# Kernel optimization log

Hardware: AMD Instinct MI355X
Metric: run time of the kernel (lower is better)

The kernel has to match this reference:

```python
import jax
import jax.numpy as jnp
import numpy as np

# Module configuration (matches init_kwargs)
N, C, H, W = 8, 256, 64, 64
CO, KH, KW = 256, 3, 3
SH, SW = 1, 1
PH, PW = 1, 1
DH, DW = 1, 1
G, DG = 1, 1
K = KH * KW
HO = (H + 2 * PH - (DH * (KH - 1) + 1)) // SH + 1
WO = (W + 2 * PW - (DW * (KW - 1) + 1)) // SW + 1


def setup_inputs() -> dict:
    key = jax.random.key(0)
    k1, k2, k3, k4 = jax.random.split(key, 4)
    x = jax.random.normal(k1, (N, C, H, W), dtype=jnp.float32)
    offset = jax.random.normal(k2, (N, DG * 2 * K, HO, WO), dtype=jnp.float32)
    mask = jax.random.uniform(k3, (N, DG * K, HO, WO), dtype=jnp.float32)
    stdv = 1.0 / np.sqrt(C * KH * KW)
    weight = jax.random.uniform(k4, (CO, C // G, KH, KW), dtype=jnp.float32,
                                minval=-stdv, maxval=stdv)
    return {"x": x, "offset": offset, "mask": mask, "weight": weight}


def _deform_sample(x, offset, mask):
    """Modulated deformable bilinear sampling (DCNv2 im2col).

    Returns columns [N, C, K, HO, WO].
    """
    Cg = C // DG
    # offset layout: [N, DG, K, 2(y,x), HO, WO]
    off = offset.reshape(N, DG, K, 2, HO, WO)
    off_y, off_x = off[:, :, :, 0], off[:, :, :, 1]

    # Base sampling grid per kernel tap: [K, HO, WO] broadcastable
    kgy = (jnp.repeat(jnp.arange(KH), KW) * DH).astype(jnp.float32)  # [K]
    kgx = (jnp.tile(jnp.arange(KW), KH) * DW).astype(jnp.float32)    # [K]
    oy = (jnp.arange(HO) * SH - PH).astype(jnp.float32)              # [HO]
    ox = (jnp.arange(WO) * SW - PW).astype(jnp.float32)              # [WO]
    py = kgy[:, None, None] + oy[None, :, None] + off_y  # [N,DG,K,HO,WO]
    px = kgx[:, None, None] + ox[None, None, :] + off_x  # [N,DG,K,HO,WO]

    y0 = jnp.floor(py)
    x0 = jnp.floor(px)
    ly = py - y0
    lx = px - x0
    y0i = y0.astype(jnp.int32)
    x0i = x0.astype(jnp.int32)
    y1i = y0i + 1
    x1i = x0i + 1

    xf = x.reshape(N, DG, Cg, H * W)

    def gather_one(xf_nd, idx_nd):
        # xf_nd: [Cg, H*W], idx_nd: [K*HO*WO] -> [Cg, K*HO*WO]
        return xf_nd[:, idx_nd]

    gather = jax.vmap(jax.vmap(gather_one))  # over N, DG

    def corner(yi, xi, wgt):
        valid = (yi >= 0) & (yi < H) & (xi >= 0) & (xi < W)
        yc = jnp.clip(yi, 0, H - 1)
        xc = jnp.clip(xi, 0, W - 1)
        idx = (yc * W + xc).reshape(N, DG, K * HO * WO)
        g = gather(xf, idx).reshape(N, DG, Cg, K, HO, WO)
        w = (wgt * valid.astype(x.dtype))[:, :, None]  # [N,DG,1,K,HO,WO]
        return g * w

    cols = corner(y0i, x0i, (1.0 - ly) * (1.0 - lx))
    cols = cols + corner(y0i, x1i, (1.0 - ly) * lx)
    cols = cols + corner(y1i, x0i, ly * (1.0 - lx))
    cols = cols + corner(y1i, x1i, ly * lx)

    # modulation
    m = mask.reshape(N, DG, 1, K, HO, WO)
    cols = cols * m
    return cols.reshape(N, C, K, HO, WO)


def reference(x, offset, mask, weight):
    cols = _deform_sample(x, offset, mask)              # [N,C,K,HO,WO]
    colsg = cols.reshape(N, G, C // G, K, HO, WO)
    wg = weight.reshape(G, CO // G, C // G, K)
    out = jnp.einsum('ngckhw,gock->ngohw', colsg, wg)
    return out.reshape(N, CO, HO, WO)
```

## Files before the change

kernel.cpp:

```cpp
#include <hip/hip_runtime.h>
#include <hip/hip_bf16.h>
#include <stdint.h>

#define N_   8
#define C_   256
#define H_   64
#define W_   64
#define CO_  256
#define K_   9
#define HO_  64
#define WO_  64
#define CK_  (C_ * K_)
#define P_   (HO_ * WO_)

#define BN   64
#define BK   64
#define NT   36
#define NTHR 512

typedef __attribute__((ext_vector_type(8))) short bf16x8;
typedef __attribute__((ext_vector_type(4))) float f32x4;

__device__ __forceinline__ unsigned short f2bf(float f) {
    uint32_t u = __builtin_bit_cast(uint32_t, f);
    uint32_t r = (u + 0x7FFFu + ((u >> 16) & 1u)) >> 16;
    return (unsigned short)r;
}
__device__ __forceinline__ float bf2f(unsigned short u) {
    return __builtin_bit_cast(float, (uint32_t)u << 16);
}
__device__ __forceinline__ float h2f(unsigned short u) {
    return (float)__builtin_bit_cast(_Float16, u);
}
__device__ __forceinline__ unsigned short f2h(float f) {
    return __builtin_bit_cast(unsigned short, (_Float16)f);
}


__global__ __launch_bounds__(256)
void transpose_x(const float* __restrict__ x, unsigned short* __restrict__ xT) {
    __shared__ float t[64][65];
    const int n  = blockIdx.z;
    const int c0 = blockIdx.y * 64;
    const int h0 = blockIdx.x * 64;
    const int tx = threadIdx.x & 63;
    const int ty = threadIdx.x >> 6;
    const float* xp = x + ((size_t)n * C_ + c0) * P_ + h0;
    #pragma unroll
    for (int i = 0; i < 16; ++i) {
        int c = ty * 16 + i;
        t[c][tx] = xp[(size_t)c * P_ + tx];
    }
    __syncthreads();
    unsigned short* op = xT + ((size_t)n * P_ + h0) * C_ + c0;
    #pragma unroll
    for (int i = 0; i < 16; ++i) {
        int hw = ty * 16 + i;
        op[(size_t)hw * C_ + tx] = f2bf(t[tx][hw]);
    }
}

__global__ __launch_bounds__(256)
void reorder_w(const float* __restrict__ w, unsigned short* __restrict__ Wt) {
    const int co = blockIdx.x;
    const int c  = threadIdx.x;
    const float* src = w + (size_t)co * CK_ + (size_t)c * K_;
    float v[9];
    #pragma unroll
    for (int k = 0; k < 9; ++k) v[k] = src[k];
    #pragma unroll
    for (int k = 0; k < 9; ++k)
        Wt[(size_t)co * CK_ + k * C_ + c] = f2bf(v[k]);
}

__device__ __forceinline__ void barrier_lgkm_only() {
    __builtin_amdgcn_sched_barrier(0);
    asm volatile("s_waitcnt lgkmcnt(0)" ::: "memory");
    __builtin_amdgcn_s_barrier();
    __builtin_amdgcn_sched_barrier(0);
}

__global__ __launch_bounds__(NTHR, 4)
void dcn_main(const unsigned short* __restrict__ xT,
              const unsigned short* __restrict__ Wt,
              const float* __restrict__ offset,
              const float* __restrict__ mask,
              float* __restrict__ out) {
    __shared__ uint2  sIdx[BN * K_];
    __shared__ uint2  sW  [BN * K_];
    __shared__ unsigned short sWs[CO_ * BK];
    __shared__ unsigned short sBs[BN * BK];

    const int tid = threadIdx.x;
    const int bid = blockIdx.x;
    const int n   = bid & 7;
    const int p0  = (bid >> 3) * BN;

    for (int e = tid; e < BN * K_; e += NTHR) {
        int pl = e / K_;
        int k  = e - pl * K_;
        int p  = p0 + pl;
        int ho = p >> 6, wo = p & 63;
        float offy = offset[(size_t)((n * 2 * K_ + 2 * k)     * P_) + p];
        float offx = offset[(size_t)((n * 2 * K_ + 2 * k + 1) * P_) + p];
        float m    = mask  [(size_t)((n * K_ + k) * P_) + p];
        float py = (float)(k / 3 + ho - 1) + offy;
        float px = (float)(k % 3 + wo - 1) + offx;
        float y0f = floorf(py), x0f = floorf(px);
        float ly = py - y0f,   lx = px - x0f;
        int y0 = (int)y0f, x0 = (int)x0f;
        int y1 = y0 + 1,   x1 = x0 + 1;
        bool vy0 = (y0 >= 0) & (y0 < H_);
        bool vy1 = (y1 >= 0) & (y1 < H_);
        bool vx0 = (x0 >= 0) & (x0 < W_);
        bool vx1 = (x1 >= 0) & (x1 < W_);
        float w00 = (1.f - ly) * (1.f - lx) * m * ((vy0 & vx0) ? 1.f : 0.f);
        float w01 = (1.f - ly) * lx         * m * ((vy0 & vx1) ? 1.f : 0.f);
        float w10 = ly * (1.f - lx)         * m * ((vy1 & vx0) ? 1.f : 0.f);
        float w11 = ly * lx                 * m * ((vy1 & vx1) ? 1.f : 0.f);
        unsigned int cy0 = (unsigned)min(max(y0, 0), H_ - 1);
        unsigned int cy1 = (unsigned)min(max(y1, 0), H_ - 1);
        unsigned int cx0 = (unsigned)min(max(x0, 0), W_ - 1);
        unsigned int cx1 = (unsigned)min(max(x1, 0), W_ - 1);
        sIdx[e] = make_uint2((cy0 * W_ + cx0) | ((cy0 * W_ + cx1) << 16),
                             (cy1 * W_ + cx0) | ((cy1 * W_ + cx1) << 16));
        sW[e]   = make_uint2((unsigned)f2h(w00) | ((unsigned)f2h(w01) << 16),
                             (unsigned)f2h(w10) | ((unsigned)f2h(w11) << 16));
    }
    __syncthreads();

    const unsigned short* xTn = xT + (size_t)n * P_ * C_;

    const int spl = tid >> 3;
    const int cs8 = (tid & 7) * 8;
    char* bdst = (char*)sBs + spl * 128 + ((((tid & 7)) ^ (spl & 7)) << 4);
    const int wco  = tid >> 1;
    const int wchq = (tid & 1) * 4;
    const int wswz = wco & 7;
    char* wrow = (char*)sWs + wco * 128;
    const unsigned short* wsrcbase = Wt + (size_t)wco * CK_ + (tid & 1) * 32;

    const int lane = tid & 63;
    const int wid  = tid >> 6;
    const int wm   = (wid & 3) * 64;
    const int wp   = (wid >> 2) * 32;
    const int l15  = lane & 15;
    const int l4   = lane >> 4;
    const int slA  = l4 ^ (l15 & 7);

    f32x4 acc[4][2] = {};

    uint4 qa, qb, qc, qd;
    uint4 wq0, wq1, wq2, wq3;

    {
        const unsigned short* ws = wsrcbase;
        wq0 = *(const uint4*)(ws);
        wq1 = *(const uint4*)(ws + 8);
        wq2 = *(const uint4*)(ws + 16);
        wq3 = *(const uint4*)(ws + 24);
        uint2 id = sIdx[spl * K_];
        const unsigned short* base = xTn + cs8;
        qa = *(const uint4*)(base + ((size_t)(id.x & 0xFFFFu) << 8));
        qb = *(const uint4*)(base + ((size_t)(id.x >> 16)     << 8));
        qc = *(const uint4*)(base + ((size_t)(id.y & 0xFFFFu) << 8));
        qd = *(const uint4*)(base + ((size_t)(id.y >> 16)     << 8));
    }

    for (int t = 0; t < NT; ++t) {
        const int k = t >> 2;

        barrier_lgkm_only();

        asm volatile("s_waitcnt vmcnt(0)" ::: "memory");

        {
            *(uint4*)(wrow + (((wchq + 0) ^ wswz) << 4)) = wq0;
            *(uint4*)(wrow + (((wchq + 1) ^ wswz) << 4)) = wq1;
            *(uint4*)(wrow + (((wchq + 2) ^ wswz) << 4)) = wq2;
            *(uint4*)(wrow + (((wchq + 3) ^ wswz) << 4)) = wq3;

            uint2 wv = sW[spl * K_ + k];
            float w0 = h2f((unsigned short)(wv.x & 0xFFFF));
            float w1 = h2f((unsigned short)(wv.x >> 16));
            float w2 = h2f((unsigned short)(wv.y & 0xFFFF));
            float w3 = h2f((unsigned short)(wv.y >> 16));
            const unsigned* pa = (const unsigned*)&qa;
            const unsigned* pb = (const unsigned*)&qb;
            const unsigned* pc = (const unsigned*)&qc;
            const unsigned* pd = (const unsigned*)&qd;
            unsigned rr[4];
            #pragma unroll
            for (int h = 0; h < 4; ++h) {
                unsigned ua = pa[h], ub = pb[h], uc = pc[h], ud = pd[h];
                float v0 = w0 * bf2f((unsigned short)(ua & 0xFFFF))
                         + w1 * bf2f((unsigned short)(ub & 0xFFFF))
                         + w2 * bf2f((unsigned short)(uc & 0xFFFF))
                         + w3 * bf2f((unsigned short)(ud & 0xFFFF));
                float v1 = w0 * bf2f((unsigned short)(ua >> 16))
                         + w1 * bf2f((unsigned short)(ub >> 16))
                         + w2 * bf2f((unsigned short)(uc >> 16))
                         + w3 * bf2f((unsigned short)(ud >> 16));
                asm("v_cvt_pk_bf16_f32 %0, %1, %2" : "=v"(rr[h]) : "v"(v0), "v"(v1));
            }
            *(uint4*)bdst = make_uint4(rr[0], rr[1], rr[2], rr[3]);
        }

        if (t + 1 < NT) {
            const int kn  = (t + 1) >> 2;
            const int c0n = ((t + 1) & 3) * 64;
            const unsigned short* ws = wsrcbase + kn * C_ + c0n;
            wq0 = *(const uint4*)(ws);
            wq1 = *(const uint4*)(ws + 8);
            wq2 = *(const uint4*)(ws + 16);
            wq3 = *(const uint4*)(ws + 24);
            uint2 id = sIdx[spl * K_ + kn];
            const unsigned short* base = xTn + c0n + cs8;
            qa = *(const uint4*)(base + ((size_t)(id.x & 0xFFFFu) << 8));
            qb = *(const uint4*)(base + ((size_t)(id.x >> 16)     << 8));
            qc = *(const uint4*)(base + ((size_t)(id.y & 0xFFFFu) << 8));
            qd = *(const uint4*)(base + ((size_t)(id.y >> 16)     << 8));
        }

        barrier_lgkm_only();

        #pragma unroll
        for (int ks = 0; ks < 2; ++ks) {
            const int sl = slA ^ (ks << 2);
            bf16x8 b0 = *(const bf16x8*)((const char*)sBs + (wp      + l15) * 128 + (sl << 4));
            bf16x8 b1 = *(const bf16x8*)((const char*)sBs + (wp + 16 + l15) * 128 + (sl << 4));
            #pragma unroll
            for (int m = 0; m < 4; ++m) {
                bf16x8 a = *(const bf16x8*)((const char*)sWs + (wm + m * 16 + l15) * 128 + (sl << 4));
                acc[m][0] = __builtin_amdgcn_mfma_f32_16x16x32_bf16(a, b0, acc[m][0], 0, 0, 0);
                acc[m][1] = __builtin_amdgcn_mfma_f32_16x16x32_bf16(a, b1, acc[m][1], 0, 0, 0);
            }
        }
    }

    float* outn = out + (size_t)n * CO_ * P_;
    #pragma unroll
    for (int m = 0; m < 4; ++m) {
        int co = wm + m * 16 + l4 * 4;
        #pragma unroll
        for (int nn = 0; nn < 2; ++nn) {
            int p = p0 + wp + nn * 16 + l15;
            #pragma unroll
            for (int r = 0; r < 4; ++r) {
                outn[(size_t)(co + r) * P_ + p] = acc[m][nn][r];
            }
        }
    }
}

template <int TAG>
__global__ __launch_bounds__(512, 2)
void dcn_fb(const float* __restrict__ x,
            const float* __restrict__ offset,
            const float* __restrict__ mask,
            const float* __restrict__ weight,
            float* __restrict__ out) {
    __shared__ uint2  sIdx[128 * K_];
    __shared__ float4 sW  [128 * K_];
    __shared__ unsigned short sWs[CO_ * 32];
    __shared__ unsigned short sBs[128 * 32];

    const int tid = threadIdx.x;
    const int n  = blockIdx.y;
    const int p0 = blockIdx.x * 128;

    for (int e = tid; e < 128 * K_; e += 512) {
        int pl = e / K_;
        int k  = e - pl * K_;
        int p  = p0 + pl;
        int ho = p >> 6, wo = p & 63;
        float offy = offset[(size_t)((n * 2 * K_ + 2 * k)     * P_) + p];
        float offx = offset[(size_t)((n * 2 * K_ + 2 * k + 1) * P_) + p];
        float m    = mask  [(size_t)((n * K_ + k) * P_) + p];
        float py = (float)(k / 3 + ho - 1) + offy;
        float px = (float)(k % 3 + wo - 1) + offx;
        float y0f = floorf(py), x0f = floorf(px);
        float ly = py - y0f,   lx = px - x0f;
        int y0 = (int)y0f, x0 = (int)x0f;
        int y1 = y0 + 1,   x1 = x0 + 1;
        bool vy0 = (y0 >= 0) & (y0 < H_);
        bool vy1 = (y1 >= 0) & (y1 < H_);
        bool vx0 = (x0 >= 0) & (x0 < W_);
        bool vx1 = (x1 >= 0) & (x1 < W_);
        float w00 = (1.f - ly) * (1.f - lx) * m * ((vy0 & vx0) ? 1.f : 0.f);
        float w01 = (1.f - ly) * lx         * m * ((vy0 & vx1) ? 1.f : 0.f);
        float w10 = ly * (1.f - lx)         * m * ((vy1 & vx0) ? 1.f : 0.f);
        float w11 = ly * lx                 * m * ((vy1 & vx1) ? 1.f : 0.f);
        unsigned int cy0 = (unsigned)min(max(y0, 0), H_ - 1);
        unsigned int cy1 = (unsigned)min(max(y1, 0), H_ - 1);
        unsigned int cx0 = (unsigned)min(max(x0, 0), W_ - 1);
        unsigned int cx1 = (unsigned)min(max(x1, 0), W_ - 1);
        sIdx[e] = make_uint2((cy0 * W_ + cx0) | ((cy0 * W_ + cx1) << 16),
                             (cy1 * W_ + cx0) | ((cy1 * W_ + cx1) << 16));
        sW[e]   = make_float4(w00, w01, w10, w11);
    }

    const float* xn = x + (size_t)n * C_ * P_;
    const int pl   = tid >> 2;
    const int pl9  = pl * K_;
    const int ckb  = (tid & 3) * 8;
    const int wco  = tid >> 1;
    const int wck  = (tid & 1) * 16;

    const int lane = tid & 63;
    const int wid  = tid >> 6;
    const int wm   = (wid & 1) * 128;
    const int wp   = (wid >> 1) * 32;
    const int l15  = lane & 15;
    const int l4   = lane >> 4;

    f32x4 acc[8][2] = {};

    for (int ck0 = 0; ck0 < CK_; ck0 += 32) {
        __syncthreads();
        {
            const float4* wsrc = (const float4*)(weight + (size_t)wco * CK_ + ck0 + wck);
            float4 wa = wsrc[0], wb = wsrc[1], wc = wsrc[2], wd = wsrc[3];
            uint4 q0, q1;
            q0.x = f2bf(wa.x) | ((unsigned)f2bf(wa.y) << 16);
            q0.y = f2bf(wa.z) | ((unsigned)f2bf(wa.w) << 16);
            q0.z = f2bf(wb.x) | ((unsigned)f2bf(wb.y) << 16);
            q0.w = f2bf(wb.z) | ((unsigned)f2bf(wb.w) << 16);
            q1.x = f2bf(wc.x) | ((unsigned)f2bf(wc.y) << 16);
            q1.y = f2bf(wc.z) | ((unsigned)f2bf(wc.w) << 16);
            q1.z = f2bf(wd.x) | ((unsigned)f2bf(wd.y) << 16);
            q1.w = f2bf(wd.z) | ((unsigned)f2bf(wd.w) << 16);
            *(uint4*)&sWs[wco * 32 + wck]     = q0;
            *(uint4*)&sWs[wco * 32 + wck + 8] = q1;
        }
        {
            int ckstart = ck0 + ckb;
            int cc = ckstart / 9;
            int kk = ckstart - cc * 9;
            unsigned int packed[4];
            unsigned short colv[8];
            #pragma unroll
            for (int j = 0; j < 8; ++j) {
                int e = pl9 + kk;
                uint2  id = sIdx[e];
                float4 wv = sW[e];
                const float* xp = xn + ((size_t)cc << 12);
                float v = wv.x * xp[id.x & 0xFFFFu]
                        + wv.y * xp[id.x >> 16]
                        + wv.z * xp[id.y & 0xFFFFu]
                        + wv.w * xp[id.y >> 16];
                colv[j] = f2bf(v);
                ++kk; if (kk == 9) { kk = 0; ++cc; }
            }
            packed[0] = colv[0] | ((unsigned)colv[1] << 16);
            packed[1] = colv[2] | ((unsigned)colv[3] << 16);
            packed[2] = colv[4] | ((unsigned)colv[5] << 16);
            packed[3] = colv[6] | ((unsigned)colv[7] << 16);
            *(uint4*)&sBs[pl * 32 + ckb] = *(uint4*)packed;
        }
        __syncthreads();
        bf16x8 bfr0 = *(const bf16x8*)&sBs[(wp + l15)      * 32 + l4 * 8];
        bf16x8 bfr1 = *(const bf16x8*)&sBs[(wp + 16 + l15) * 32 + l4 * 8];
        #pragma unroll
        for (int m = 0; m < 8; ++m) {
            bf16x8 afr = *(const bf16x8*)&sWs[(wm + m * 16 + l15) * 32 + l4 * 8];
            acc[m][0] = __builtin_amdgcn_mfma_f32_16x16x32_bf16(afr, bfr0, acc[m][0], 0, 0, 0);
            acc[m][1] = __builtin_amdgcn_mfma_f32_16x16x32_bf16(afr, bfr1, acc[m][1], 0, 0, 0);
        }
    }

    float* outn = out + (size_t)n * CO_ * P_;
    #pragma unroll
    for (int m = 0; m < 8; ++m) {
        int co = wm + m * 16 + l4 * 4;
        #pragma unroll
        for (int nn = 0; nn < 2; ++nn) {
            int p = p0 + wp + nn * 16 + l15;
            #pragma unroll
            for (int r = 0; r < 4; ++r) {
                outn[(size_t)(co + r) * P_ + p] = acc[m][nn][r];
            }
        }
    }
}

extern "C" void kernel_launch(void* const* d_in, const int* in_sizes, int n_in,
                              void* d_out, int out_size, void* d_ws, size_t ws_size,
                              hipStream_t stream) {
    const float* x      = (const float*)d_in[0];
    const float* offset = (const float*)d_in[1];
    const float* mask   = (const float*)d_in[2];
    const float* weight = (const float*)d_in[3];
    float* out = (float*)d_out;

    const size_t xT_elems = (size_t)N_ * P_ * C_;
    const size_t Wt_elems = (size_t)CO_ * CK_;
    const size_t need     = (xT_elems + Wt_elems) * sizeof(unsigned short);

    if (ws_size >= need) {
        unsigned short* xT = (unsigned short*)d_ws;
        unsigned short* Wt = xT + xT_elems;
        transpose_x<<<dim3(P_ / 64, C_ / 64, N_), dim3(256), 0, stream>>>(x, xT);
        reorder_w<<<dim3(CO_), dim3(256), 0, stream>>>(weight, Wt);
        dcn_main<<<dim3((P_ / BN) * N_), dim3(NTHR), 0, stream>>>(xT, Wt, offset, mask, out);
    } else if (ws_size >= (8u << 20)) {
        dcn_fb<1><<<dim3(P_ / 128, N_), dim3(512), 0, stream>>>(x, offset, mask, weight, out);
    } else {
        dcn_fb<0><<<dim3(P_ / 128, N_), dim3(512), 0, stream>>>(x, offset, mask, weight, out);
    }
}
```

Baseline: 83.59 us.

## Switch main path to fp16 with packed half2 bilinear math and split output channels

Converts the transposed input and reordered weights to fp16 instead of bf16. The bilinear interpolation now uses packed half2 multiply-adds rather than scalar fp32 math, and the GEMM uses f16 MFMA. Each block now covers 128 output channels instead of 256, which doubles the grid and raises the occupancy hint to 8. In exchange, each block pair repeats the sampling/gather work for its pixels, and accumulating interpolation in fp16 reduces precision.

```diff
diff --git a/kernel.cpp b/kernel.cpp
--- a/kernel.cpp
+++ b/kernel.cpp
@@ -1,5 +1,6 @@
 #include <hip/hip_runtime.h>
 #include <hip/hip_bf16.h>
+#include <hip/hip_fp16.h>
 #include <stdint.h>
 
 #define N_   8
@@ -14,11 +15,12 @@
 #define P_   (HO_ * WO_)
 
 #define BN   64
+#define BCO  128
 #define BK   64
 #define NT   36
 #define NTHR 512
 
-typedef __attribute__((ext_vector_type(8))) short bf16x8;
+typedef __attribute__((ext_vector_type(8))) _Float16 f16x8;
 typedef __attribute__((ext_vector_type(4))) float f32x4;
 
 __device__ __forceinline__ unsigned short f2bf(float f) {
@@ -26,14 +28,11 @@
     uint32_t r = (u + 0x7FFFu + ((u >> 16) & 1u)) >> 16;
     return (unsigned short)r;
 }
+__device__ __forceinline__ unsigned short f2h(float f) {
+    return __builtin_bit_cast(unsigned short, (_Float16)f);
+}
 __device__ __forceinline__ float bf2f(unsigned short u) {
     return __builtin_bit_cast(float, (uint32_t)u << 16);
-}
-__device__ __forceinline__ float h2f(unsigned short u) {
-    return (float)__builtin_bit_cast(_Float16, u);
-}
-__device__ __forceinline__ unsigned short f2h(float f) {
-    return __builtin_bit_cast(unsigned short, (_Float16)f);
 }
 
 
@@ -56,7 +55,7 @@
     #pragma unroll
     for (int i = 0; i < 16; ++i) {
         int hw = ty * 16 + i;
-        op[(size_t)hw * C_ + tx] = f2bf(t[tx][hw]);
+        op[(size_t)hw * C_ + tx] = f2h(t[tx][hw]);
     }
 }
 
@@ -70,7 +69,7 @@
     for (int k = 0; k < 9; ++k) v[k] = src[k];
     #pragma unroll
     for (int k = 0; k < 9; ++k)
-        Wt[(size_t)co * CK_ + k * C_ + c] = f2bf(v[k]);
+        Wt[(size_t)co * CK_ + k * C_ + c] = f2h(v[k]);
 }
 
 __device__ __forceinline__ void barrier_lgkm_only() {
@@ -80,21 +79,23 @@
     __builtin_amdgcn_sched_barrier(0);
 }
 
-__global__ __launch_bounds__(NTHR, 4)
+__global__ __launch_bounds__(NTHR, 8)
 void dcn_main(const unsigned short* __restrict__ xT,
               const unsigned short* __restrict__ Wt,
               const float* __restrict__ offset,
               const float* __restrict__ mask,
               float* __restrict__ out) {
-    __shared__ uint2  sIdx[BN * K_];
-    __shared__ uint2  sW  [BN * K_];
-    __shared__ unsigned short sWs[CO_ * BK];
+    __shared__ uint2 sIdx[BN * K_];
+    __shared__ uint4 sWd [BN * K_];
+    __shared__ unsigned short sWs[BCO * BK];
     __shared__ unsigned short sBs[BN * BK];
 
     const int tid = threadIdx.x;
     const int bid = blockIdx.x;
     const int n   = bid & 7;
-    const int p0  = (bid >> 3) * BN;
+    const int r   = bid >> 3;
+    const int p0  = (r >> 1) * BN;
+    const int co0 = (r & 1) * BCO;
 
     for (int e = tid; e < BN * K_; e += NTHR) {
         int pl = e / K_;
@@ -124,8 +125,10 @@
         unsigned int cx1 = (unsigned)min(max(x1, 0), W_ - 1);
         sIdx[e] = make_uint2((cy0 * W_ + cx0) | ((cy0 * W_ + cx1) << 16),
                              (cy1 * W_ + cx0) | ((cy1 * W_ + cx1) << 16));
-        sW[e]   = make_uint2((unsigned)f2h(w00) | ((unsigned)f2h(w01) << 16),
-                             (unsigned)f2h(w10) | ((unsigned)f2h(w11) << 16));
+        sWd[e] = make_uint4((unsigned)f2h(w00) * 0x10001u,
+                            (unsigned)f2h(w01) * 0x10001u,
+                            (unsigned)f2h(w10) * 0x10001u,
+                            (unsigned)f2h(w11) * 0x10001u);
     }
     __syncthreads();
 
@@ -133,32 +136,30 @@
 
     const int spl = tid >> 3;
     const int cs8 = (tid & 7) * 8;
-    char* bdst = (char*)sBs + spl * 128 + ((((tid & 7)) ^ (spl & 7)) << 4);
-    const int wco  = tid >> 1;
-    const int wchq = (tid & 1) * 4;
+    char* bdst = (char*)sBs + spl * 128 + (((tid & 7) ^ (spl & 7)) << 4);
+    const int wco = tid >> 2;
+    const int wsl = tid & 3;
     const int wswz = wco & 7;
     char* wrow = (char*)sWs + wco * 128;
-    const unsigned short* wsrcbase = Wt + (size_t)wco * CK_ + (tid & 1) * 32;
+    const unsigned short* wsrcbase = Wt + (size_t)(co0 + wco) * CK_ + wsl * 8;
 
     const int lane = tid & 63;
     const int wid  = tid >> 6;
-    const int wm   = (wid & 3) * 64;
+    const int wm   = (wid & 3) * 32;
     const int wp   = (wid >> 2) * 32;
     const int l15  = lane & 15;
     const int l4   = lane >> 4;
     const int slA  = l4 ^ (l15 & 7);
 
-    f32x4 acc[4][2] = {};
+    f32x4 acc[2][2] = {};
 
     uint4 qa, qb, qc, qd;
-    uint4 wq0, wq1, wq2, wq3;
+    uint4 wq0, wq1;
 
     {
         const unsigned short* ws = wsrcbase;
         wq0 = *(const uint4*)(ws);
-        wq1 = *(const uint4*)(ws + 8);
-        wq2 = *(const uint4*)(ws + 16);
-        wq3 = *(const uint4*)(ws + 24);
+        wq1 = *(const uint4*)(ws + 32);
         uint2 id = sIdx[spl * K_];
         const unsigned short* base = xTn + cs8;
         qa = *(const uint4*)(base + ((size_t)(id.x & 0xFFFFu) << 8));
@@ -175,16 +176,14 @@
         asm volatile("s_waitcnt vmcnt(0)" ::: "memory");
 
         {
-            *(uint4*)(wrow + (((wchq + 0) ^ wswz) << 4)) = wq0;
-            *(uint4*)(wrow + (((wchq + 1) ^ wswz) << 4)) = wq1;
-            *(uint4*)(wrow + (((wchq + 2) ^ wswz) << 4)) = wq2;
-            *(uint4*)(wrow + (((wchq + 3) ^ wswz) << 4)) = wq3;
-
-            uint2 wv = sW[spl * K_ + k];
-            float w0 = h2f((unsigned short)(wv.x & 0xFFFF));
-            float w1 = h2f((unsigned short)(wv.x >> 16));
-            float w2 = h2f((unsigned short)(wv.y & 0xFFFF));
-            float w3 = h2f((unsigned short)(wv.y >> 16));
+            *(uint4*)(wrow + ((wsl       ^ wswz) << 4)) = wq0;
+            *(uint4*)(wrow + (((wsl + 4) ^ wswz) << 4)) = wq1;
+
+            uint4 wv = sWd[spl * K_ + k];
+            __half2 W0 = __builtin_bit_cast(__half2, wv.x);
+            __half2 W1 = __builtin_bit_cast(__half2, wv.y);
+            __half2 W2 = __builtin_bit_cast(__half2, wv.z);
+            __half2 W3 = __builtin_bit_cast(__half2, wv.w);
             const unsigned* pa = (const unsigned*)&qa;
             const unsigned* pb = (const unsigned*)&qb;
             const unsigned* pc = (const unsigned*)&qc;
@@ -192,16 +191,11 @@
             unsigned rr[4];
             #pragma unroll
             for (int h = 0; h < 4; ++h) {
-                unsigned ua = pa[h], ub = pb[h], uc = pc[h], ud = pd[h];
-                float v0 = w0 * bf2f((unsigned short)(ua & 0xFFFF))
-                         + w1 * bf2f((unsigned short)(ub & 0xFFFF))
-                         + w2 * bf2f((unsigned short)(uc & 0xFFFF))
-                         + w3 * bf2f((unsigned short)(ud & 0xFFFF));
-                float v1 = w0 * bf2f((unsigned short)(ua >> 16))
-                         + w1 * bf2f((unsigned short)(ub >> 16))
-                         + w2 * bf2f((unsigned short)(uc >> 16))
-                         + w3 * bf2f((unsigned short)(ud >> 16));
-                asm("v_cvt_pk_bf16_f32 %0, %1, %2" : "=v"(rr[h]) : "v"(v0), "v"(v1));
+                __half2 v = __hmul2(W0, __builtin_bit_cast(__half2, pa[h]));
+                v = __hfma2(W1, __builtin_bit_cast(__half2, pb[h]), v);
+                v = __hfma2(W2, __builtin_bit_cast(__half2, pc[h]), v);
+                v = __hfma2(W3, __builtin_bit_cast(__half2, pd[h]), v);
+                rr[h] = __builtin_bit_cast(unsigned, v);
             }
             *(uint4*)bdst = make_uint4(rr[0], rr[1], rr[2], rr[3]);
         }
@@ -211,9 +205,7 @@
             const int c0n = ((t + 1) & 3) * 64;
             const unsigned short* ws = wsrcbase + kn * C_ + c0n;
             wq0 = *(const uint4*)(ws);
-            wq1 = *(const uint4*)(ws + 8);
-            wq2 = *(const uint4*)(ws + 16);
-            wq3 = *(const uint4*)(ws + 24);
+            wq1 = *(const uint4*)(ws + 32);
             uint2 id = sIdx[spl * K_ + kn];
             const unsigned short* base = xTn + c0n + cs8;
             qa = *(const uint4*)(base + ((size_t)(id.x & 0xFFFFu) << 8));
@@ -227,27 +219,27 @@
         #pragma unroll
         for (int ks = 0; ks < 2; ++ks) {
             const int sl = slA ^ (ks << 2);
-            bf16x8 b0 = *(const bf16x8*)((const char*)sBs + (wp      + l15) * 128 + (sl << 4));
-            bf16x8 b1 = *(const bf16x8*)((const char*)sBs + (wp + 16 + l15) * 128 + (sl << 4));
+            f16x8 b0 = *(const f16x8*)((const char*)sBs + (wp      + l15) * 128 + (sl << 4));
+            f16x8 b1 = *(const f16x8*)((const char*)sBs + (wp + 16 + l15) * 128 + (sl << 4));
             #pragma unroll
-            for (int m = 0; m < 4; ++m) {
-                bf16x8 a = *(const bf16x8*)((const char*)sWs + (wm + m * 16 + l15) * 128 + (sl << 4));
-                acc[m][0] = __builtin_amdgcn_mfma_f32_16x16x32_bf16(a, b0, acc[m][0], 0, 0, 0);
-                acc[m][1] = __builtin_amdgcn_mfma_f32_16x16x32_bf16(a, b1, acc[m][1], 0, 0, 0);
+            for (int m = 0; m < 2; ++m) {
+                f16x8 a = *(const f16x8*)((const char*)sWs + (wm + m * 16 + l15) * 128 + (sl << 4));
+                acc[m][0] = __builtin_amdgcn_mfma_f32_16x16x32_f16(a, b0, acc[m][0], 0, 0, 0);
+                acc[m][1] = __builtin_amdgcn_mfma_f32_16x16x32_f16(a, b1, acc[m][1], 0, 0, 0);
             }
         }
     }
 
     float* outn = out + (size_t)n * CO_ * P_;
     #pragma unroll
-    for (int m = 0; m < 4; ++m) {
-        int co = wm + m * 16 + l4 * 4;
+    for (int m = 0; m < 2; ++m) {
+        int co = co0 + wm + m * 16 + l4 * 4;
         #pragma unroll
         for (int nn = 0; nn < 2; ++nn) {
             int p = p0 + wp + nn * 16 + l15;
             #pragma unroll
-            for (int r = 0; r < 4; ++r) {
-                outn[(size_t)(co + r) * P_ + p] = acc[m][nn][r];
+            for (int rr = 0; rr < 4; ++rr) {
+                outn[(size_t)(co + rr) * P_ + p] = acc[m][nn][rr];
             }
         }
     }
@@ -260,6 +252,7 @@
             const float* __restrict__ mask,
             const float* __restrict__ weight,
             float* __restrict__ out) {
+    typedef __attribute__((ext_vector_type(8))) short bf16x8;
     __shared__ uint2  sIdx[128 * K_];
     __shared__ float4 sW  [128 * K_];
     __shared__ unsigned short sWs[CO_ * 32];
@@ -377,8 +370,8 @@
         for (int nn = 0; nn < 2; ++nn) {
             int p = p0 + wp + nn * 16 + l15;
             #pragma unroll
-            for (int r = 0; r < 4; ++r) {
-                outn[(size_t)(co + r) * P_ + p] = acc[m][nn][r];
+            for (int rr = 0; rr < 4; ++rr) {
+                outn[(size_t)(co + rr) * P_ + p] = acc[m][nn][rr];
             }
         }
     }
@@ -402,7 +395,7 @@
         unsigned short* Wt = xT + xT_elems;
         transpose_x<<<dim3(P_ / 64, C_ / 64, N_), dim3(256), 0, stream>>>(x, xT);
         reorder_w<<<dim3(CO_), dim3(256), 0, stream>>>(weight, Wt);
-        dcn_main<<<dim3((P_ / BN) * N_), dim3(NTHR), 0, stream>>>(xT, Wt, offset, mask, out);
+        dcn_main<<<dim3((P_ / BN) * (CO_ / BCO) * N_), dim3(NTHR), 0, stream>>>(xT, Wt, offset, mask, out);
     } else if (ws_size >= (8u << 20)) {
         dcn_fb<1><<<dim3(P_ / 128, N_), dim3(512), 0, stream>>>(x, offset, mask, weight, out);
     } else {
```

Result: slower. 116.6 us (+39.5%).
